# Performance work log

Measured on AMD Instinct MI355X. Metric: run time of the kernel, lower is better.

The kernel has to match this reference:

```python
import jax, jax.numpy as jnp
import numpy as np

B, S, NX, NH = 4, 1024, 1024, 16
HD = NX // NH  # head_features = 64


def setup_inputs() -> dict:
    key = jax.random.key(0)
    k1, k2, k3 = jax.random.split(key, 3)
    x = jax.random.normal(k1, (B, S, NX), dtype=jnp.float32)
    w_attn = 0.02 * jax.random.normal(k2, (NX, 3 * NX), dtype=jnp.float32)
    b_attn = jnp.zeros((3 * NX,), dtype=jnp.float32)
    w_proj = 0.02 * jax.random.normal(k3, (NX, NX), dtype=jnp.float32)
    b_proj = jnp.zeros((NX,), dtype=jnp.float32)
    causal_bias = jnp.tril(jnp.ones((S, S), dtype=jnp.float32))  # tril buffer
    return {"x": x, "w_attn": w_attn, "b_attn": b_attn,
            "w_proj": w_proj, "b_proj": b_proj, "causal_bias": causal_bias}


def reference(x, w_attn, b_attn, w_proj, b_proj, causal_bias):
    # c_attn: fused qkv projection (Conv1D == addmm)
    qkv = x @ w_attn + b_attn                     # [B, S, 3*NX]
    q, k, v = jnp.split(qkv, 3, axis=-1)          # each [B, S, NX]
    # split heads -> [B, H, S, D]
    q = q.reshape(B, S, NH, HD).transpose(0, 2, 1, 3)
    k = k.reshape(B, S, NH, HD).transpose(0, 2, 1, 3)
    v = v.reshape(B, S, NH, HD).transpose(0, 2, 1, 3)
    # present: stack of (key in [B,H,S,D] layout, value)
    present = jnp.stack((k, v))                   # [2, B, H, S, D]
    # scores with scale=True
    w = jnp.einsum('bhqd,bhkd->bhqk', q, k) / jnp.sqrt(jnp.float32(HD))
    b = causal_bias[None, None, :, :]             # [1,1,S,S] (nd==ns==S)
    w = w * b - 1e10 * (1.0 - b)                  # multiplicative mask trick
    p = jax.nn.softmax(w, axis=-1)
    a = jnp.einsum('bhqk,bhkd->bhqd', p, v)       # [B, H, S, D]
    a = a.transpose(0, 2, 1, 3).reshape(B, S, NX)  # merge heads
    out = a @ w_proj + b_proj                     # c_proj
    return out, present
```

## Files before the change

kernel.cpp:

```cpp
#include <hip/hip_runtime.h>
#include <hip/hip_bf16.h>

typedef __attribute__((ext_vector_type(8))) short short8;
typedef __attribute__((ext_vector_type(4))) float floatx4;

constexpr int Bsz = 4, Ssz = 1024, NXc = 1024, NHc = 16, HDc = 64;
constexpr int OUT_ELEMS  = Bsz * Ssz * NXc;
constexpr int HEAD_ELEMS = Bsz * NHc * Ssz * HDc;

union BF8 { __hip_bfloat16 h[8]; uint4 v; short8 s; };

__device__ __forceinline__ uint4 cvt8(const float* __restrict__ p) {
    float4 a = *reinterpret_cast<const float4*>(p);
    float4 b = *reinterpret_cast<const float4*>(p + 4);
    BF8 u;
    u.h[0] = __float2bfloat16(a.x); u.h[1] = __float2bfloat16(a.y);
    u.h[2] = __float2bfloat16(a.z); u.h[3] = __float2bfloat16(a.w);
    u.h[4] = __float2bfloat16(b.x); u.h[5] = __float2bfloat16(b.y);
    u.h[6] = __float2bfloat16(b.z); u.h[7] = __float2bfloat16(b.w);
    return u.v;
}

__device__ __forceinline__ void load_lds_16B(const void* g, void* l) {
    __builtin_amdgcn_global_load_lds(
        (const __attribute__((address_space(1))) unsigned int*)g,
        (__attribute__((address_space(3))) unsigned int*)l, 16, 0, 0);
}


__global__ __launch_bounds__(256) void cvt_kernel(
    const float* __restrict__ in, __hip_bfloat16* __restrict__ out, int n)
{
    int i = (blockIdx.x * 256 + threadIdx.x) * 8;
    if (i < n)
        *reinterpret_cast<uint4*>(out + i) = cvt8(in + i);
}

__global__ __launch_bounds__(256) void transpose_cvt(
    const float* __restrict__ in, __hip_bfloat16* __restrict__ out,
    int K, int N)
{
    __shared__ float t[64][65];
    const int tid = threadIdx.x;
    const int k0 = blockIdx.y * 64, n0 = blockIdx.x * 64;
#pragma unroll
    for (int j = 0; j < 16; ++j) {
        const int idx = tid + j * 256;
        const int row = idx >> 6, col = idx & 63;
        t[row][col] = in[(size_t)(k0 + row) * N + n0 + col];
    }
    __syncthreads();
#pragma unroll
    for (int j = 0; j < 16; ++j) {
        const int idx = tid + j * 256;
        const int orow = idx >> 6, ocol = idx & 63;
        out[(size_t)(n0 + orow) * K + k0 + ocol] = __float2bfloat16(t[ocol][orow]);
    }
}

template <int EPI>
__global__ __launch_bounds__(256) void gemm128(
    const __hip_bfloat16* __restrict__ A,
    const __hip_bfloat16* __restrict__ Bt,
    const float* __restrict__ bias,
    float* __restrict__ outf,
    __hip_bfloat16* __restrict__ qws,
    float* __restrict__ present,
    int M, int N, int K)
{
    __shared__ __align__(16) __hip_bfloat16 As[128 * 32];
    __shared__ __align__(16) __hip_bfloat16 Bs[128 * 32];

    const int tid  = threadIdx.x;
    const int w    = tid >> 6, lane = tid & 63;
    const int quad = lane >> 4, l16 = lane & 15;
    const int m0 = blockIdx.y * 128, n0 = blockIdx.x * 128;
    const int mb = (w >> 1) * 64, nbw = (w & 1) * 64;

    const int srow = lane >> 2;
    const int skseg = (lane & 3) * 8;

    floatx4 acc[4][4];
#pragma unroll
    for (int i = 0; i < 4; ++i)
#pragma unroll
        for (int j = 0; j < 4; ++j)
#pragma unroll
            for (int r = 0; r < 4; ++r) acc[i][j][r] = 0.f;

    for (int k0 = 0; k0 < K; k0 += 32) {
#pragma unroll
        for (int c = 0; c < 2; ++c) {
            const int chunk = w * 2 + c;
            const int row = chunk * 16 + srow;
            load_lds_16B(A + (size_t)(m0 + row) * K + k0 + skseg,
                         &As[chunk * 512]);
            load_lds_16B(Bt + (size_t)(n0 + row) * K + k0 + skseg,
                         &Bs[chunk * 512]);
        }
        __syncthreads();

        short8 af[4], bfr[4];
#pragma unroll
        for (int mi = 0; mi < 4; ++mi)
            af[mi] = *reinterpret_cast<const short8*>(
                &As[(mb + mi * 16 + l16) * 32 + quad * 8]);
#pragma unroll
        for (int ni = 0; ni < 4; ++ni)
            bfr[ni] = *reinterpret_cast<const short8*>(
                &Bs[(nbw + ni * 16 + l16) * 32 + quad * 8]);
#pragma unroll
        for (int mi = 0; mi < 4; ++mi)
#pragma unroll
            for (int ni = 0; ni < 4; ++ni)
                acc[mi][ni] = __builtin_amdgcn_mfma_f32_16x16x32_bf16(
                    af[mi], bfr[ni], acc[mi][ni], 0, 0, 0);

        __syncthreads();
    }

#pragma unroll
    for (int mi = 0; mi < 4; ++mi) {
#pragma unroll
        for (int ni = 0; ni < 4; ++ni) {
            const int col = n0 + nbw + ni * 16 + l16;
            const float bsv = bias[col];
#pragma unroll
            for (int r = 0; r < 4; ++r) {
                const int row = m0 + mb + mi * 16 + quad * 4 + r;
                const float v = acc[mi][ni][r] + bsv;
                if (EPI == 0) {
                    const int seg = col >> 10;
                    const int c = col & 1023;
                    if (seg == 0) {
                        qws[(size_t)row * 1024 + c] = __float2bfloat16(v);
                    } else {
                        const int b = row >> 10, s = row & 1023;
                        const int h = c >> 6, d = c & 63;
                        const size_t idx =
                            ((size_t)((b * 16 + h) * 1024 + s)) * 64 + d;
                        if (seg == 1) present[idx] = v;
                        else          present[HEAD_ELEMS + idx] = v;
                    }
                } else {
                    outf[(size_t)row * N + col] = v;
                }
            }
        }
    }
}

__global__ __launch_bounds__(256) void attn_v2(
    const __hip_bfloat16* __restrict__ qws,
    const float* __restrict__ present,
    __hip_bfloat16* __restrict__ a_ws)
{
    const int bx = blockIdx.x, h = blockIdx.y, b = blockIdx.z;
    const int tid  = threadIdx.x;
    const int wave = tid >> 6, lane = tid & 63;
    const int quad = lane >> 4, l16 = lane & 15;
    const int stripe = wave * 16;

    const size_t headoff = ((size_t)(b * 16 + h)) * Ssz * HDc;
    const float* Kp = present + headoff;
    const float* Vp = present + HEAD_ELEMS + headoff;

    __shared__ __align__(16) __hip_bfloat16 Ks[64][72];
    __shared__ __align__(16) __hip_bfloat16 Vts[64][72];
    __shared__ __align__(16) __hip_bfloat16 Ps[64][72];

    const int krow = tid >> 3, kseg = tid & 7;
    const int vd = tid & 63, vg = tid >> 6;

#pragma unroll
    for (int pass = 0; pass < 2; ++pass) {
        const int qt = (pass == 0) ? (8 + bx) : (7 - bx);

        const __hip_bfloat16* Qb =
            qws + ((size_t)(b * Ssz + qt * 64 + stripe + l16)) * NXc + h * 64;
        short8 qf0 = *reinterpret_cast<const short8*>(Qb + quad * 8);
        short8 qf1 = *reinterpret_cast<const short8*>(Qb + 32 + quad * 8);

        float m_i[4], l_i[4];
#pragma unroll
        for (int r = 0; r < 4; ++r) { m_i[r] = -1e9f; l_i[r] = 0.f; }
        floatx4 oacc[4];
#pragma unroll
        for (int ni = 0; ni < 4; ++ni)
#pragma unroll
            for (int r = 0; r < 4; ++r) oacc[ni][r] = 0.f;

        for (int kt = 0; kt <= qt; ++kt) {
#pragma unroll
            for (int it = 0; it < 2; ++it) {
                const int kr = krow + it * 32;
                *reinterpret_cast<uint4*>(&Ks[kr][kseg * 8]) =
                    cvt8(Kp + (size_t)(kt * 64 + kr) * 64 + kseg * 8);

                const int kb = (it * 4 + vg) * 8;
                BF8 u;
#pragma unroll
                for (int i = 0; i < 8; ++i)
                    u.h[i] = __float2bfloat16(
                        Vp[(size_t)(kt * 64 + kb + i) * 64 + vd]);
                *reinterpret_cast<uint4*>(&Vts[vd][kb]) = u.v;
            }
            __syncthreads();

            floatx4 sacc[4];
#pragma unroll
            for (int ni = 0; ni < 4; ++ni)
#pragma unroll
                for (int r = 0; r < 4; ++r) sacc[ni][r] = 0.f;
#pragma unroll
            for (int ni = 0; ni < 4; ++ni) {
                short8 kf0 = *reinterpret_cast<const short8*>(
                    &Ks[ni * 16 + l16][quad * 8]);
                short8 kf1 = *reinterpret_cast<const short8*>(
                    &Ks[ni * 16 + l16][32 + quad * 8]);
                sacc[ni] = __builtin_amdgcn_mfma_f32_16x16x32_bf16(
                    qf0, kf0, sacc[ni], 0, 0, 0);
                sacc[ni] = __builtin_amdgcn_mfma_f32_16x16x32_bf16(
                    qf1, kf1, sacc[ni], 0, 0, 0);
            }

            const bool diag = (kt == qt);
            float alpha_[4];
#pragma unroll
            for (int r = 0; r < 4; ++r) {
                const int lrow = stripe + quad * 4 + r;
                float sv[4];
                float mx = -1e30f;
#pragma unroll
                for (int ni = 0; ni < 4; ++ni) {
                    float v = sacc[ni][r] * 0.125f;
                    if (diag && (ni * 16 + l16) > lrow) v = -1e9f;
                    sv[ni] = v;
                    mx = fmaxf(mx, v);
                }
                mx = fmaxf(mx, __shfl_xor(mx, 1));
                mx = fmaxf(mx, __shfl_xor(mx, 2));
                mx = fmaxf(mx, __shfl_xor(mx, 4));
                mx = fmaxf(mx, __shfl_xor(mx, 8));
                const float mnew = fmaxf(m_i[r], mx);
                const float al = __expf(m_i[r] - mnew);
                m_i[r] = mnew;
                float s = 0.f;
#pragma unroll
                for (int nn = 0; nn < 4; ++nn) {
                    const int ni = (nn + quad) & 3;
                    const float p = __expf(sv[ni] - mnew);
                    s += p;
                    Ps[lrow][ni * 16 + l16] = __float2bfloat16(p);
                }
                s += __shfl_xor(s, 1);
                s += __shfl_xor(s, 2);
                s += __shfl_xor(s, 4);
                s += __shfl_xor(s, 8);
                l_i[r] = l_i[r] * al + s;
                alpha_[r] = al;
            }

#pragma unroll
            for (int ni = 0; ni < 4; ++ni)
#pragma unroll
                for (int r = 0; r < 4; ++r) oacc[ni][r] *= alpha_[r];

#pragma unroll
            for (int kk = 0; kk < 64; kk += 32) {
                short8 pf = *reinterpret_cast<const short8*>(
                    &Ps[stripe + l16][kk + quad * 8]);
#pragma unroll
                for (int ni = 0; ni < 4; ++ni) {
                    short8 vf = *reinterpret_cast<const short8*>(
                        &Vts[ni * 16 + l16][kk + quad * 8]);
                    oacc[ni] = __builtin_amdgcn_mfma_f32_16x16x32_bf16(
                        pf, vf, oacc[ni], 0, 0, 0);
                }
            }
            __syncthreads();
        }

#pragma unroll
        for (int ni = 0; ni < 4; ++ni) {
#pragma unroll
            for (int r = 0; r < 4; ++r) {
                const int row = qt * 64 + stripe + quad * 4 + r;
                const int col = h * 64 + ni * 16 + l16;
                const float inv = 1.0f / fmaxf(l_i[r], 1e-20f);
                a_ws[((size_t)(b * Ssz + row)) * NXc + col] =
                    __float2bfloat16(oacc[ni][r] * inv);
            }
        }
    }
}

template <int EPI>
__global__ __launch_bounds__(256) void gemm64(
    const void* __restrict__ Av, const float* __restrict__ Bw,
    const float* __restrict__ bias, float* __restrict__ out0,
    float* __restrict__ present, int M, int N, int K)
{
    __shared__ __align__(16) __hip_bfloat16 As[64][40];
    __shared__ __align__(16) __hip_bfloat16 Bs[64][40];
    const int tid = threadIdx.x;
    const int wave = tid >> 6, lane = tid & 63;
    const int quad = lane >> 4, l16 = lane & 15;
    const int m0 = blockIdx.y * 64, n0 = blockIdx.x * 64;
    const int mb = (wave >> 1) * 32, nb = (wave & 1) * 32;
    const int arow = tid >> 2, aseg = tid & 3;
    const int brow = tid >> 3, bseg = tid & 7;
    floatx4 acc[2][2];
#pragma unroll
    for (int i = 0; i < 2; ++i)
#pragma unroll
        for (int j = 0; j < 2; ++j)
#pragma unroll
            for (int r = 0; r < 4; ++r) acc[i][j][r] = 0.f;
    for (int k0 = 0; k0 < K; k0 += 32) {
        if (EPI == 0) {
            const float* A = (const float*)Av;
            *reinterpret_cast<uint4*>(&As[arow][aseg * 8]) =
                cvt8(A + (size_t)(m0 + arow) * K + k0 + aseg * 8);
        } else {
            const __hip_bfloat16* A = (const __hip_bfloat16*)Av;
            *reinterpret_cast<uint4*>(&As[arow][aseg * 8]) =
                *reinterpret_cast<const uint4*>(
                    A + (size_t)(m0 + arow) * K + k0 + aseg * 8);
        }
        const float* bp = Bw + (size_t)(k0 + brow) * N + n0 + bseg * 8;
        float4 b0 = *reinterpret_cast<const float4*>(bp);
        float4 b1 = *reinterpret_cast<const float4*>(bp + 4);
        Bs[bseg * 8 + 0][brow] = __float2bfloat16(b0.x);
        Bs[bseg * 8 + 1][brow] = __float2bfloat16(b0.y);
        Bs[bseg * 8 + 2][brow] = __float2bfloat16(b0.z);
        Bs[bseg * 8 + 3][brow] = __float2bfloat16(b0.w);
        Bs[bseg * 8 + 4][brow] = __float2bfloat16(b1.x);
        Bs[bseg * 8 + 5][brow] = __float2bfloat16(b1.y);
        Bs[bseg * 8 + 6][brow] = __float2bfloat16(b1.z);
        Bs[bseg * 8 + 7][brow] = __float2bfloat16(b1.w);
        __syncthreads();
        short8 af[2], bf[2];
#pragma unroll
        for (int mm = 0; mm < 2; ++mm)
            af[mm] = *reinterpret_cast<const short8*>(&As[mb + mm * 16 + l16][quad * 8]);
#pragma unroll
        for (int nn = 0; nn < 2; ++nn)
            bf[nn] = *reinterpret_cast<const short8*>(&Bs[nb + nn * 16 + l16][quad * 8]);
#pragma unroll
        for (int mm = 0; mm < 2; ++mm)
#pragma unroll
            for (int nn = 0; nn < 2; ++nn)
                acc[mm][nn] = __builtin_amdgcn_mfma_f32_16x16x32_bf16(
                    af[mm], bf[nn], acc[mm][nn], 0, 0, 0);
        __syncthreads();
    }
#pragma unroll
    for (int mm = 0; mm < 2; ++mm)
#pragma unroll
        for (int nn = 0; nn < 2; ++nn) {
            const int col = n0 + nb + nn * 16 + l16;
            const float bsv = bias[col];
#pragma unroll
            for (int r = 0; r < 4; ++r) {
                const int row = m0 + mb + mm * 16 + quad * 4 + r;
                const float v = acc[mm][nn][r] + bsv;
                if (EPI == 0) {
                    const int seg = col >> 10;
                    const int c = col & 1023;
                    if (seg == 0) out0[(size_t)row * 1024 + c] = v;
                    else {
                        const int b = row >> 10, s = row & 1023;
                        const int h = c >> 6, d = c & 63;
                        const size_t idx = ((size_t)((b * 16 + h) * 1024 + s)) * 64 + d;
                        if (seg == 1) present[idx] = v;
                        else          present[HEAD_ELEMS + idx] = v;
                    }
                } else out0[(size_t)row * N + col] = v;
            }
        }
}

__global__ __launch_bounds__(256) void attn64(
    const float* __restrict__ qbuf, const float* __restrict__ present,
    __hip_bfloat16* __restrict__ a_ws)
{
    const int qt = blockIdx.x, h = blockIdx.y, b = blockIdx.z;
    const int tid = threadIdx.x;
    const int wave = tid >> 6, lane = tid & 63;
    const int quad = lane >> 4, l16 = lane & 15;
    const int mb = (wave >> 1) * 32, nb = (wave & 1) * 32;
    const size_t headoff = ((size_t)(b * 16 + h)) * Ssz * HDc;
    const float* Qb = qbuf + ((size_t)(b * Ssz + qt * 64)) * NXc + h * 64;
    const float* Kp = present + headoff;
    const float* Vp = present + HEAD_ELEMS + headoff;
    __shared__ __align__(16) __hip_bfloat16 Qs[64][72];
    __shared__ __align__(16) __hip_bfloat16 Ks[64][72];
    __shared__ __align__(16) __hip_bfloat16 Vts[64][72];
    __shared__ __align__(16) __hip_bfloat16 Ps[64][72];
    __shared__ float Sc[64][65];
    __shared__ float mrow[64], lrow[64], arw[64];
#pragma unroll
    for (int it = 0; it < 2; ++it) {
        const int c = tid + it * 256;
        const int row = c >> 3, seg = c & 7;
        *reinterpret_cast<uint4*>(&Qs[row][seg * 8]) =
            cvt8(Qb + (size_t)row * NXc + seg * 8);
    }
    if (tid < 64) { mrow[tid] = -1e9f; lrow[tid] = 0.f; }
    floatx4 oacc[2][2];
#pragma unroll
    for (int i = 0; i < 2; ++i)
#pragma unroll
        for (int j = 0; j < 2; ++j)
#pragma unroll
            for (int r = 0; r < 4; ++r) oacc[i][j][r] = 0.f;
    __syncthreads();
    for (int kt = 0; kt <= qt; ++kt) {
#pragma unroll
        for (int it = 0; it < 2; ++it) {
            const int c = tid + it * 256;
            const int row = c >> 3, seg = c & 7;
            *reinterpret_cast<uint4*>(&Ks[row][seg * 8]) =
                cvt8(Kp + (size_t)(kt * 64 + row) * 64 + seg * 8);
            const float* vp = Vp + (size_t)(kt * 64 + row) * 64 + seg * 8;
            float4 v0 = *reinterpret_cast<const float4*>(vp);
            float4 v1 = *reinterpret_cast<const float4*>(vp + 4);
            Vts[seg * 8 + 0][row] = __float2bfloat16(v0.x);
            Vts[seg * 8 + 1][row] = __float2bfloat16(v0.y);
            Vts[seg * 8 + 2][row] = __float2bfloat16(v0.z);
            Vts[seg * 8 + 3][row] = __float2bfloat16(v0.w);
            Vts[seg * 8 + 4][row] = __float2bfloat16(v1.x);
            Vts[seg * 8 + 5][row] = __float2bfloat16(v1.y);
            Vts[seg * 8 + 6][row] = __float2bfloat16(v1.z);
            Vts[seg * 8 + 7][row] = __float2bfloat16(v1.w);
        }
        __syncthreads();
        floatx4 sacc[2][2];
#pragma unroll
        for (int i = 0; i < 2; ++i)
#pragma unroll
            for (int j = 0; j < 2; ++j)
#pragma unroll
                for (int r = 0; r < 4; ++r) sacc[i][j][r] = 0.f;
#pragma unroll
        for (int kd = 0; kd < 64; kd += 32) {
            short8 af[2], bf[2];
#pragma unroll
            for (int mm = 0; mm < 2; ++mm)
                af[mm] = *reinterpret_cast<const short8*>(&Qs[mb + mm * 16 + l16][kd + quad * 8]);
#pragma unroll
            for (int nn = 0; nn < 2; ++nn)
                bf[nn] = *reinterpret_cast<const short8*>(&Ks[nb + nn * 16 + l16][kd + quad * 8]);
#pragma unroll
            for (int mm = 0; mm < 2; ++mm)
#pragma unroll
                for (int nn = 0; nn < 2; ++nn)
                    sacc[mm][nn] = __builtin_amdgcn_mfma_f32_16x16x32_bf16(
                        af[mm], bf[nn], sacc[mm][nn], 0, 0, 0);
        }
        const bool diag = (kt == qt);
#pragma unroll
        for (int mm = 0; mm < 2; ++mm)
#pragma unroll
            for (int nn = 0; nn < 2; ++nn)
#pragma unroll
                for (int r = 0; r < 4; ++r) {
                    const int row = mb + mm * 16 + quad * 4 + r;
                    const int col = nb + nn * 16 + l16;
                    float v = fminf(fmaxf(sacc[mm][nn][r] * 0.125f, -1e8f), 1e8f);
                    if (diag && col > row) v = -1e9f;
                    Sc[row][col] = v;
                }
        __syncthreads();
        if (tid < 64) {
            const int r = tid;
            const float mo = mrow[r];
            float mx = mo;
            for (int c = 0; c < 64; ++c) mx = fmaxf(mx, Sc[r][c]);
            const float al = (mo <= -5e8f) ? 0.f : __expf(mo - mx);
            float sum = 0.f;
            for (int c = 0; c < 64; ++c) {
                const float sv = Sc[r][c];
                const float p = (sv <= -5e8f) ? 0.f : __expf(sv - mx);
                sum += p;
                Ps[r][c] = __float2bfloat16(p);
            }
            mrow[r] = mx;
            lrow[r] = lrow[r] * al + sum;
            arw[r]  = al;
        }
        __syncthreads();
#pragma unroll
        for (int mm = 0; mm < 2; ++mm) {
            const int rbase = mb + mm * 16 + quad * 4;
#pragma unroll
            for (int r = 0; r < 4; ++r) {
                const float al = arw[rbase + r];
                oacc[mm][0][r] *= al;
                oacc[mm][1][r] *= al;
            }
        }
#pragma unroll
        for (int kk = 0; kk < 64; kk += 32) {
            short8 pf[2], vf[2];
#pragma unroll
            for (int mm = 0; mm < 2; ++mm)
                pf[mm] = *reinterpret_cast<const short8*>(&Ps[mb + mm * 16 + l16][kk + quad * 8]);
#pragma unroll
            for (int nn = 0; nn < 2; ++nn)
                vf[nn] = *reinterpret_cast<const short8*>(&Vts[nb + nn * 16 + l16][kk + quad * 8]);
#pragma unroll
            for (int mm = 0; mm < 2; ++mm)
#pragma unroll
                for (int nn = 0; nn < 2; ++nn)
                    oacc[mm][nn] = __builtin_amdgcn_mfma_f32_16x16x32_bf16(
                        pf[mm], vf[nn], oacc[mm][nn], 0, 0, 0);
        }
        __syncthreads();
    }
#pragma unroll
    for (int mm = 0; mm < 2; ++mm)
#pragma unroll
        for (int nn = 0; nn < 2; ++nn)
#pragma unroll
            for (int r = 0; r < 4; ++r) {
                const int row = mb + mm * 16 + quad * 4 + r;
                const int col = nb + nn * 16 + l16;
                const float inv = 1.0f / fmaxf(lrow[row], 1e-20f);
                a_ws[((size_t)(b * Ssz + qt * 64 + row)) * NXc + h * 64 + col] =
                    __float2bfloat16(oacc[mm][nn][r] * inv);
            }
}

extern "C" void kernel_launch(void* const* d_in, const int* in_sizes, int n_in,
                              void* d_out, int out_size, void* d_ws, size_t ws_size,
                              hipStream_t stream) {
    const float* x      = (const float*)d_in[0];
    const float* w_attn = (const float*)d_in[1];
    const float* b_attn = (const float*)d_in[2];
    const float* w_proj = (const float*)d_in[3];
    const float* b_proj = (const float*)d_in[4];

    float* out     = (float*)d_out;
    float* present = out + OUT_ELEMS;

    const size_t NEED = 32u * 1024u * 1024u;
    if (ws_size >= NEED) {
        __hip_bfloat16* a_ws = (__hip_bfloat16*)d_ws;
        __hip_bfloat16* q_ws = a_ws + 4194304;
        __hip_bfloat16* x_bf = q_ws + 4194304;
        __hip_bfloat16* wTa  = x_bf + 4194304;
        __hip_bfloat16* wTp  = wTa + 3145728;

        cvt_kernel<<<2048, 256, 0, stream>>>(x, x_bf, OUT_ELEMS);
        transpose_cvt<<<dim3(48, 16), 256, 0, stream>>>(w_attn, wTa, 1024, 3072);
        transpose_cvt<<<dim3(16, 16), 256, 0, stream>>>(w_proj, wTp, 1024, 1024);

        gemm128<0><<<dim3(24, 32), 256, 0, stream>>>(
            x_bf, wTa, b_attn, nullptr, q_ws, present, 4096, 3072, 1024);

        attn_v2<<<dim3(8, 16, 4), 256, 0, stream>>>(q_ws, present, a_ws);

        gemm128<1><<<dim3(8, 32), 256, 0, stream>>>(
            a_ws, wTp, b_proj, out, nullptr, nullptr, 4096, 1024, 1024);
    } else {
        __hip_bfloat16* a_ws = (__hip_bfloat16*)d_ws;
        hipMemsetAsync(d_ws, 0, (size_t)OUT_ELEMS * sizeof(__hip_bfloat16), stream);
        gemm64<0><<<dim3(48, 64), 256, 0, stream>>>(x, w_attn, b_attn, out, present,
                                                    4096, 3072, 1024);
        attn64<<<dim3(16, 16, 4), 256, 0, stream>>>(out, present, a_ws);
        gemm64<1><<<dim3(16, 64), 256, 0, stream>>>(a_ws, w_proj, b_proj, out, nullptr,
                                                    4096, 1024, 1024);
    }
}
```

Baseline: 230.4 us.

## Pre-pack K and transposed V to swizzled bf16 tiles and stream them into LDS

Adds a repack kernel that converts K from fp32 to bf16 once, and transposes V through shared memory, into 64x64 XOR-swizzled tiles in workspace. The attention kernel then moves those tiles into LDS with direct global-to-LDS loads, reading from matching swizzled offsets. Previously every query tile re-converted fp32 K and gathered V with strided loads. The grid also changes from paired query tiles per block to one tile per block, ordered heaviest first, and workspace regions are reused (V^T in the old x buffer, output written over Q). The cost is an extra kernel launch and another pass over K/V in memory.

New measurement: 244.2 us. +6.0%, slower.

```diff
diff --git a/kernel.cpp b/kernel.cpp
--- a/kernel.cpp
+++ b/kernel.cpp
@@ -150,147 +150,180 @@
     }
 }
 
-__global__ __launch_bounds__(256) void attn_v2(
-    const __hip_bfloat16* __restrict__ qws,
+__global__ __launch_bounds__(256) void repack_kv(
     const float* __restrict__ present,
+    __hip_bfloat16* __restrict__ k_ws,
+    __hip_bfloat16* __restrict__ vt_ws)
+{
+    const int kt = blockIdx.x;
+    const int bh = blockIdx.y;
+    const int tid = threadIdx.x;
+    const size_t toff = ((size_t)bh * 1024 + kt * 64) * 64;
+    const float* Kp = present + toff;
+    const float* Vp = present + HEAD_ELEMS + toff;
+    __hip_bfloat16* ko = k_ws  + ((size_t)bh * 16 + kt) * 4096;
+    __hip_bfloat16* vo = vt_ws + ((size_t)bh * 16 + kt) * 4096;
+
+    __shared__ float Vt[64][65];
+
+    const int row = tid >> 3, seg = tid & 7;
+#pragma unroll
+    for (int it = 0; it < 2; ++it) {
+        const int r = row + it * 32;
+        *reinterpret_cast<uint4*>(&ko[r * 64 + ((seg ^ (r & 7)) << 3)]) =
+            cvt8(Kp + (size_t)r * 64 + seg * 8);
+        const float* vp = Vp + (size_t)r * 64 + seg * 8;
+        float4 v0 = *reinterpret_cast<const float4*>(vp);
+        float4 v1 = *reinterpret_cast<const float4*>(vp + 4);
+        Vt[seg * 8 + 0][r] = v0.x; Vt[seg * 8 + 1][r] = v0.y;
+        Vt[seg * 8 + 2][r] = v0.z; Vt[seg * 8 + 3][r] = v0.w;
+        Vt[seg * 8 + 4][r] = v1.x; Vt[seg * 8 + 5][r] = v1.y;
+        Vt[seg * 8 + 6][r] = v1.z; Vt[seg * 8 + 7][r] = v1.w;
+    }
+    __syncthreads();
+#pragma unroll
+    for (int it = 0; it < 2; ++it) {
+        const int d = row + it * 32;
+        BF8 u;
+#pragma unroll
+        for (int i = 0; i < 8; ++i)
+            u.h[i] = __float2bfloat16(Vt[d][seg * 8 + i]);
+        *reinterpret_cast<uint4*>(&vo[d * 64 + ((seg ^ (d & 7)) << 3)]) = u.v;
+    }
+}
+
+__global__ __launch_bounds__(256) void attn_v3(
+    const __hip_bfloat16* __restrict__ q_ws,
+    const __hip_bfloat16* __restrict__ k_ws,
+    const __hip_bfloat16* __restrict__ vt_ws,
     __hip_bfloat16* __restrict__ a_ws)
 {
-    const int bx = blockIdx.x, h = blockIdx.y, b = blockIdx.z;
+    const int qt = 15 - blockIdx.x, h = blockIdx.y, b = blockIdx.z;
     const int tid  = threadIdx.x;
     const int wave = tid >> 6, lane = tid & 63;
     const int quad = lane >> 4, l16 = lane & 15;
     const int stripe = wave * 16;
 
-    const size_t headoff = ((size_t)(b * 16 + h)) * Ssz * HDc;
-    const float* Kp = present + headoff;
-    const float* Vp = present + HEAD_ELEMS + headoff;
-
-    __shared__ __align__(16) __hip_bfloat16 Ks[64][72];
-    __shared__ __align__(16) __hip_bfloat16 Vts[64][72];
+    const int bh = b * 16 + h;
+    const __hip_bfloat16* Kbase = k_ws  + (size_t)bh * 16 * 4096;
+    const __hip_bfloat16* Vbase = vt_ws + (size_t)bh * 16 * 4096;
+
+    __shared__ __align__(16) __hip_bfloat16 Ksf[4096];
+    __shared__ __align__(16) __hip_bfloat16 Vsf[4096];
     __shared__ __align__(16) __hip_bfloat16 Ps[64][72];
 
-    const int krow = tid >> 3, kseg = tid & 7;
-    const int vd = tid & 63, vg = tid >> 6;
-
-#pragma unroll
-    for (int pass = 0; pass < 2; ++pass) {
-        const int qt = (pass == 0) ? (8 + bx) : (7 - bx);
-
-        const __hip_bfloat16* Qb =
-            qws + ((size_t)(b * Ssz + qt * 64 + stripe + l16)) * NXc + h * 64;
-        short8 qf0 = *reinterpret_cast<const short8*>(Qb + quad * 8);
-        short8 qf1 = *reinterpret_cast<const short8*>(Qb + 32 + quad * 8);
-
-        float m_i[4], l_i[4];
-#pragma unroll
-        for (int r = 0; r < 4; ++r) { m_i[r] = -1e9f; l_i[r] = 0.f; }
-        floatx4 oacc[4];
+    const __hip_bfloat16* Qb =
+        q_ws + ((size_t)(b * Ssz + qt * 64 + stripe + l16)) * NXc + h * 64;
+    const short8 qf0 = *reinterpret_cast<const short8*>(Qb + quad * 8);
+    const short8 qf1 = *reinterpret_cast<const short8*>(Qb + 32 + quad * 8);
+
+    float m_i[4], l_i[4];
+#pragma unroll
+    for (int r = 0; r < 4; ++r) { m_i[r] = -1e9f; l_i[r] = 0.f; }
+    floatx4 oacc[4];
+#pragma unroll
+    for (int ni = 0; ni < 4; ++ni)
+#pragma unroll
+        for (int r = 0; r < 4; ++r) oacc[ni][r] = 0.f;
+
+    for (int kt = 0; kt <= qt; ++kt) {
+        const __hip_bfloat16* Kt = Kbase + kt * 4096;
+        const __hip_bfloat16* Vt = Vbase + kt * 4096;
+#pragma unroll
+        for (int c2 = 0; c2 < 2; ++c2) {
+            const int c = wave + c2 * 4;
+            load_lds_16B(Kt + c * 512 + (lane << 3), &Ksf[c * 512]);
+            load_lds_16B(Vt + c * 512 + (lane << 3), &Vsf[c * 512]);
+        }
+        __syncthreads();
+
+        floatx4 sacc[4];
 #pragma unroll
         for (int ni = 0; ni < 4; ++ni)
 #pragma unroll
-            for (int r = 0; r < 4; ++r) oacc[ni][r] = 0.f;
-
-        for (int kt = 0; kt <= qt; ++kt) {
-#pragma unroll
-            for (int it = 0; it < 2; ++it) {
-                const int kr = krow + it * 32;
-                *reinterpret_cast<uint4*>(&Ks[kr][kseg * 8]) =
-                    cvt8(Kp + (size_t)(kt * 64 + kr) * 64 + kseg * 8);
-
-                const int kb = (it * 4 + vg) * 8;
-                BF8 u;
-#pragma unroll
-                for (int i = 0; i < 8; ++i)
-                    u.h[i] = __float2bfloat16(
-                        Vp[(size_t)(kt * 64 + kb + i) * 64 + vd]);
-                *reinterpret_cast<uint4*>(&Vts[vd][kb]) = u.v;
-            }
-            __syncthreads();
-
-            floatx4 sacc[4];
-#pragma unroll
-            for (int ni = 0; ni < 4; ++ni)
-#pragma unroll
-                for (int r = 0; r < 4; ++r) sacc[ni][r] = 0.f;
+            for (int r = 0; r < 4; ++r) sacc[ni][r] = 0.f;
+#pragma unroll
+        for (int ni = 0; ni < 4; ++ni) {
+            const int key = ni * 16 + l16;
+            const int sw = key & 7;
+            const short8 kf0 = *reinterpret_cast<const short8*>(
+                &Ksf[key * 64 + ((quad ^ sw) << 3)]);
+            const short8 kf1 = *reinterpret_cast<const short8*>(
+                &Ksf[key * 64 + (((4 + quad) ^ sw) << 3)]);
+            sacc[ni] = __builtin_amdgcn_mfma_f32_16x16x32_bf16(
+                qf0, kf0, sacc[ni], 0, 0, 0);
+            sacc[ni] = __builtin_amdgcn_mfma_f32_16x16x32_bf16(
+                qf1, kf1, sacc[ni], 0, 0, 0);
+        }
+
+        const bool diag = (kt == qt);
+        float alpha_[4];
+#pragma unroll
+        for (int r = 0; r < 4; ++r) {
+            const int lrow = stripe + quad * 4 + r;
+            float sv[4];
+            float mx = -1e30f;
 #pragma unroll
             for (int ni = 0; ni < 4; ++ni) {
-                short8 kf0 = *reinterpret_cast<const short8*>(
-                    &Ks[ni * 16 + l16][quad * 8]);
-                short8 kf1 = *reinterpret_cast<const short8*>(
-                    &Ks[ni * 16 + l16][32 + quad * 8]);
-                sacc[ni] = __builtin_amdgcn_mfma_f32_16x16x32_bf16(
-                    qf0, kf0, sacc[ni], 0, 0, 0);
-                sacc[ni] = __builtin_amdgcn_mfma_f32_16x16x32_bf16(
-                    qf1, kf1, sacc[ni], 0, 0, 0);
-            }
-
-            const bool diag = (kt == qt);
-            float alpha_[4];
-#pragma unroll
-            for (int r = 0; r < 4; ++r) {
-                const int lrow = stripe + quad * 4 + r;
-                float sv[4];
-                float mx = -1e30f;
-#pragma unroll
-                for (int ni = 0; ni < 4; ++ni) {
-                    float v = sacc[ni][r] * 0.125f;
-                    if (diag && (ni * 16 + l16) > lrow) v = -1e9f;
-                    sv[ni] = v;
-                    mx = fmaxf(mx, v);
-                }
-                mx = fmaxf(mx, __shfl_xor(mx, 1));
-                mx = fmaxf(mx, __shfl_xor(mx, 2));
-                mx = fmaxf(mx, __shfl_xor(mx, 4));
-                mx = fmaxf(mx, __shfl_xor(mx, 8));
-                const float mnew = fmaxf(m_i[r], mx);
-                const float al = __expf(m_i[r] - mnew);
-                m_i[r] = mnew;
-                float s = 0.f;
-#pragma unroll
-                for (int nn = 0; nn < 4; ++nn) {
-                    const int ni = (nn + quad) & 3;
-                    const float p = __expf(sv[ni] - mnew);
-                    s += p;
-                    Ps[lrow][ni * 16 + l16] = __float2bfloat16(p);
-                }
-                s += __shfl_xor(s, 1);
-                s += __shfl_xor(s, 2);
-                s += __shfl_xor(s, 4);
-                s += __shfl_xor(s, 8);
-                l_i[r] = l_i[r] * al + s;
-                alpha_[r] = al;
-            }
-
-#pragma unroll
-            for (int ni = 0; ni < 4; ++ni)
-#pragma unroll
-                for (int r = 0; r < 4; ++r) oacc[ni][r] *= alpha_[r];
-
-#pragma unroll
-            for (int kk = 0; kk < 64; kk += 32) {
-                short8 pf = *reinterpret_cast<const short8*>(
-                    &Ps[stripe + l16][kk + quad * 8]);
-#pragma unroll
-                for (int ni = 0; ni < 4; ++ni) {
-                    short8 vf = *reinterpret_cast<const short8*>(
-                        &Vts[ni * 16 + l16][kk + quad * 8]);
-                    oacc[ni] = __builtin_amdgcn_mfma_f32_16x16x32_bf16(
-                        pf, vf, oacc[ni], 0, 0, 0);
-                }
-            }
-            __syncthreads();
-        }
-
-#pragma unroll
-        for (int ni = 0; ni < 4; ++ni) {
-#pragma unroll
-            for (int r = 0; r < 4; ++r) {
-                const int row = qt * 64 + stripe + quad * 4 + r;
-                const int col = h * 64 + ni * 16 + l16;
-                const float inv = 1.0f / fmaxf(l_i[r], 1e-20f);
-                a_ws[((size_t)(b * Ssz + row)) * NXc + col] =
-                    __float2bfloat16(oacc[ni][r] * inv);
-            }
+                float v = sacc[ni][r] * 0.125f;
+                if (diag && (ni * 16 + l16) > lrow) v = -1e9f;
+                sv[ni] = v;
+                mx = fmaxf(mx, v);
+            }
+            mx = fmaxf(mx, __shfl_xor(mx, 1));
+            mx = fmaxf(mx, __shfl_xor(mx, 2));
+            mx = fmaxf(mx, __shfl_xor(mx, 4));
+            mx = fmaxf(mx, __shfl_xor(mx, 8));
+            const float mnew = fmaxf(m_i[r], mx);
+            const float al = __expf(m_i[r] - mnew);
+            m_i[r] = mnew;
+            float s = 0.f;
+#pragma unroll
+            for (int nn = 0; nn < 4; ++nn) {
+                const int ni = (nn + quad) & 3;
+                const float p = __expf(sv[ni] - mnew);
+                s += p;
+                Ps[lrow][ni * 16 + l16] = __float2bfloat16(p);
+            }
+            s += __shfl_xor(s, 1);
+            s += __shfl_xor(s, 2);
+            s += __shfl_xor(s, 4);
+            s += __shfl_xor(s, 8);
+            l_i[r] = l_i[r] * al + s;
+            alpha_[r] = al;
+        }
+
+#pragma unroll
+        for (int ni = 0; ni < 4; ++ni)
+#pragma unroll
+            for (int r = 0; r < 4; ++r) oacc[ni][r] *= alpha_[r];
+
+#pragma unroll
+        for (int kk = 0; kk < 64; kk += 32) {
+            const short8 pf = *reinterpret_cast<const short8*>(
+                &Ps[stripe + l16][kk + quad * 8]);
+#pragma unroll
+            for (int ni = 0; ni < 4; ++ni) {
+                const int d = ni * 16 + l16;
+                const int chunk = (kk >> 3) + quad;
+                const short8 vf = *reinterpret_cast<const short8*>(
+                    &Vsf[d * 64 + ((chunk ^ (d & 7)) << 3)]);
+                oacc[ni] = __builtin_amdgcn_mfma_f32_16x16x32_bf16(
+                    pf, vf, oacc[ni], 0, 0, 0);
+            }
+        }
+        __syncthreads();
+    }
+
+#pragma unroll
+    for (int ni = 0; ni < 4; ++ni) {
+#pragma unroll
+        for (int r = 0; r < 4; ++r) {
+            const int row = qt * 64 + stripe + quad * 4 + r;
+            const int col = h * 64 + ni * 16 + l16;
+            const float inv = 1.0f / fmaxf(l_i[r], 1e-20f);
+            a_ws[((size_t)(b * Ssz + row)) * NXc + col] =
+                __float2bfloat16(oacc[ni][r] * inv);
         }
     }
 }
@@ -547,23 +580,25 @@
 
     const size_t NEED = 32u * 1024u * 1024u;
     if (ws_size >= NEED) {
-        __hip_bfloat16* a_ws = (__hip_bfloat16*)d_ws;
-        __hip_bfloat16* q_ws = a_ws + 4194304;
-        __hip_bfloat16* x_bf = q_ws + 4194304;
-        __hip_bfloat16* wTa  = x_bf + 4194304;
+        __hip_bfloat16* reg1 = (__hip_bfloat16*)d_ws;
+        __hip_bfloat16* reg2 = reg1 + 4194304;
+        __hip_bfloat16* reg3 = reg2 + 4194304;
+        __hip_bfloat16* wTa  = reg3 + 4194304;
         __hip_bfloat16* wTp  = wTa + 3145728;
 
-        cvt_kernel<<<2048, 256, 0, stream>>>(x, x_bf, OUT_ELEMS);
+        cvt_kernel<<<2048, 256, 0, stream>>>(x, reg1, OUT_ELEMS);
         transpose_cvt<<<dim3(48, 16), 256, 0, stream>>>(w_attn, wTa, 1024, 3072);
         transpose_cvt<<<dim3(16, 16), 256, 0, stream>>>(w_proj, wTp, 1024, 1024);
 
         gemm128<0><<<dim3(24, 32), 256, 0, stream>>>(
-            x_bf, wTa, b_attn, nullptr, q_ws, present, 4096, 3072, 1024);
-
-        attn_v2<<<dim3(8, 16, 4), 256, 0, stream>>>(q_ws, present, a_ws);
+            reg1, wTa, b_attn, nullptr, reg2, present, 4096, 3072, 1024);
+
+        repack_kv<<<dim3(16, 64), 256, 0, stream>>>(present, reg3, reg1);
+
+        attn_v3<<<dim3(16, 16, 4), 256, 0, stream>>>(reg2, reg3, reg1, reg2);
 
         gemm128<1><<<dim3(8, 32), 256, 0, stream>>>(
-            a_ws, wTp, b_proj, out, nullptr, nullptr, 4096, 1024, 1024);
+            reg2, wTp, b_proj, out, nullptr, nullptr, 4096, 1024, 1024);
     } else {
         __hip_bfloat16* a_ws = (__hip_bfloat16*)d_ws;
         hipMemsetAsync(d_ws, 0, (size_t)OUT_ELEMS * sizeof(__hip_bfloat16), stream);
```
